# Optimization experiments

Hardware: AMD Instinct MI355X
Metric: run time of the kernel (lower is better)

The kernel has to match this reference:

```python
import jax, jax.numpy as jnp
import numpy as np

LEAK = 0.95
THRESHOLD = 1.0
CLAMP = 3.0
LN_EPS = 1e-5


def setup_inputs() -> dict:
    key = jax.random.key(0)
    k1, k2 = jax.random.split(key)
    B, S, V, D = 8, 2048, 57344, 1536
    token_ids = jax.random.randint(k1, (B, S), 0, V, dtype=jnp.int64)
    emb_table = jax.random.normal(k2, (V, D), dtype=jnp.float32) * 0.02
    gamma = jnp.ones((D,), dtype=jnp.float32)
    beta = jnp.zeros((D,), dtype=jnp.float32)
    return {"token_ids": token_ids, "emb_table": emb_table, "gamma": gamma, "beta": beta}


def _layernorm(x, gamma, beta):
    mu = jnp.mean(x, axis=-1, keepdims=True)
    var = jnp.mean(jnp.square(x - mu), axis=-1, keepdims=True)
    return (x - mu) * jax.lax.rsqrt(var + LN_EPS) * gamma + beta


def _lif_scan(x):
    # x: [B, S, D]; sequential LIF recurrence over time axis S
    B, S, D = x.shape
    v0 = jnp.zeros((B, D), dtype=x.dtype)

    def step(v, xt):
        v = v * LEAK + xt
        v = jnp.clip(v, -CLAMP, CLAMP)
        spike = (v >= THRESHOLD).astype(x.dtype)
        return v * (1.0 - spike), spike

    _, spikes = jax.lax.scan(step, v0, jnp.swapaxes(x, 0, 1))  # spikes: [S, B, D]
    return jnp.swapaxes(spikes, 0, 1)


def reference(token_ids, emb_table, gamma, beta):
    x = emb_table[token_ids]          # [B, S, D] embedding lookup
    x = _layernorm(x, gamma, beta)    # continuous residual stream
    spikes = _lif_scan(x)             # 0/1 spike tensor [B, S, D]
    return spikes, x
```

## Files before the change

kernel.cpp:

```cpp
#include <hip/hip_runtime.h>


constexpr int Bv = 8, Sv = 2048, Dv = 1536;
constexpr int Cn = 16;
constexpr int Ln = Sv / Cn;
constexpr int Wn = 64;
constexpr int BD = Bv * Dv;
constexpr int TNMAX = Ln + Wn;

constexpr size_t FLAG_OFF  = 0;
constexpr size_t STATS_OFF = 64;
constexpr size_t SPEC0_OFF = STATS_OFF + (size_t)2 * Bv * Sv * 8;
constexpr size_t SPEC1_OFF = SPEC0_OFF + (size_t)Cn * BD * 8;
constexpr size_t WS_NEED   = SPEC1_OFF + (size_t)Cn * BD * 8;

__device__ __forceinline__ double ln_x64(float e, double mu, double rs,
                                         double gd, double bd) {
#pragma clang fp contract(off)
    return (((double)e - mu) * rs) * gd + bd;
}
__device__ __forceinline__ double lif_step(double v, double x, bool& spike) {
#pragma clang fp contract(off)
    double vv = v * 0.95;
    vv = vv + x;
    vv = fmin(fmax(vv, -3.0), 3.0);
    spike = (vv >= 1.0);
    return spike ? 0.0 : vv;
}

extern "C" __global__ __launch_bounds__(256)
void detect_tok64(const int* __restrict__ tok, int* __restrict__ flag)
{
    __shared__ int any_nz;
    if (threadIdx.x == 0) any_nz = 0;
    __syncthreads();
    int nz = 0;
    for (int i = threadIdx.x; i < (Bv * Sv) / 2; i += 256) nz |= tok[2 * i + 1];
    if (nz) atomicOr(&any_nz, 1);
    __syncthreads();
    if (threadIdx.x == 0) flag[0] = (any_nz == 0) ? 1 : 0;
}

extern "C" __global__ __launch_bounds__(128)
void ln_stats_kernel(const int* __restrict__ tok,
                     const float* __restrict__ emb,
                     const float* __restrict__ gamma,
                     const float* __restrict__ beta,
                     float* __restrict__ x_out,
                     double* __restrict__ stats,
                     const int* __restrict__ tok64_flag)
{
#pragma clang fp contract(off)
    __shared__ double p1[2], p2[2];

    const int row = blockIdx.x;
    const int t   = threadIdx.x;
    const int lane = t & 63, wave = t >> 6;

    const int shift = tok64_flag[0];
    const long long tk = (long long)tok[(size_t)row << shift];
    const float* src = emb + tk * (long long)Dv;

    float4 xv[3];
#pragma unroll
    for (int k = 0; k < 3; ++k) xv[k] = reinterpret_cast<const float4*>(src)[t + 128 * k];

    double s = 0.0;
#pragma unroll
    for (int k = 0; k < 3; ++k) {
        s += (double)xv[k].x; s += (double)xv[k].y;
        s += (double)xv[k].z; s += (double)xv[k].w;
    }
#pragma unroll
    for (int off = 1; off < 64; off <<= 1) s += __shfl_xor(s, off);
    if (lane == 0) p1[wave] = s;
    __syncthreads();
    const double mu = (p1[0] + p1[1]) / 1536.0;

    double q = 0.0;
#pragma unroll
    for (int k = 0; k < 3; ++k) {
        double d0 = (double)xv[k].x - mu; q += d0 * d0;
        double d1 = (double)xv[k].y - mu; q += d1 * d1;
        double d2 = (double)xv[k].z - mu; q += d2 * d2;
        double d3 = (double)xv[k].w - mu; q += d3 * d3;
    }
#pragma unroll
    for (int off = 1; off < 64; off <<= 1) q += __shfl_xor(q, off);
    if (lane == 0) p2[wave] = q;
    __syncthreads();
    const double var  = (p2[0] + p2[1]) / 1536.0;
    const double rstd = 1.0 / sqrt(var + 1e-5);

    if (t == 0) { stats[2 * row] = mu; stats[2 * row + 1] = rstd; }

    float* dst = x_out + (long long)row * Dv;
#pragma unroll
    for (int k = 0; k < 3; ++k) {
        const int f4 = t + 128 * k;
        const float4 g4 = reinterpret_cast<const float4*>(gamma)[f4];
        const float4 b4 = reinterpret_cast<const float4*>(beta)[f4];
        float4 o;
        o.x = (float)((((double)xv[k].x - mu) * rstd) * (double)g4.x + (double)b4.x);
        o.y = (float)((((double)xv[k].y - mu) * rstd) * (double)g4.y + (double)b4.y);
        o.z = (float)((((double)xv[k].z - mu) * rstd) * (double)g4.z + (double)b4.z);
        o.w = (float)((((double)xv[k].w - mu) * rstd) * (double)g4.w + (double)b4.w);
        reinterpret_cast<float4*>(dst)[f4] = o;
    }
}

extern "C" __global__ __launch_bounds__(256)
void lif64_spec(const int* __restrict__ tok,
                const float* __restrict__ emb,
                const float* __restrict__ gamma,
                const float* __restrict__ beta,
                const double* __restrict__ stats,
                float* __restrict__ spk,
                double* __restrict__ spec_start,
                double* __restrict__ spec_end,
                const int* __restrict__ tok64_flag)
{
    constexpr int DBLK = Dv / 256;
    __shared__ int     tokl[TNMAX];
    __shared__ double2 statl[TNMAX];

    const int t    = threadIdx.x;
    const int bid  = blockIdx.x;
    const int dblk = bid % DBLK;
    const int c    = (bid / DBLK) % Cn;
    const int b    = bid / (DBLK * Cn);
    const int d    = dblk * 256 + t;

    const int s0 = c * Ln;
    const int sw = (c == 0) ? 0 : s0 - Wn;
    const int TN = s0 + Ln - sw;
    const int warm = s0 - sw;
    const int rowbase = b * Sv;

    if (t < TN) {
        const int row = rowbase + sw + t;
        const int shift = tok64_flag[0];
        tokl[t]  = tok[(size_t)row << shift];
        statl[t] = reinterpret_cast<const double2*>(stats)[row];
    }
    __syncthreads();

    const double gd = (double)gamma[d];
    const double bd = (double)beta[d];
    float* sp = spk + (size_t)b * Sv * Dv + d;

    constexpr int U = 16;
    float ecur[U], enxt[U];
#pragma unroll
    for (int k = 0; k < U; ++k)
        ecur[k] = emb[(long long)tokl[k] * Dv + d];

    double v = 0.0, vstart = 0.0;
    for (int i = 0; i < TN; i += U) {
        if (i + U < TN) {
#pragma unroll
            for (int k = 0; k < U; ++k)
                enxt[k] = emb[(long long)tokl[i + U + k] * Dv + d];
        }
#pragma unroll
        for (int k = 0; k < U; ++k) {
            const int idx = i + k;
            if (idx == warm) vstart = v;
            const double2 st = statl[idx];
            const double x = ln_x64(ecur[k], st.x, st.y, gd, bd);
            bool spike;
            const double vn = lif_step(v, x, spike);
            if (idx >= warm)
                __builtin_nontemporal_store(spike ? 1.0f : 0.0f,
                                            &sp[(size_t)(sw + idx) * Dv]);
            v = vn;
        }
#pragma unroll
        for (int k = 0; k < U; ++k) ecur[k] = enxt[k];
    }

    const size_t chain = (size_t)b * Dv + d;
    spec_start[(size_t)c * BD + chain] = vstart;
    spec_end[(size_t)c * BD + chain]   = v;
}

extern "C" __global__ __launch_bounds__(64)
void lif64_fixup(const int* __restrict__ tok,
                 const float* __restrict__ emb,
                 const float* __restrict__ gamma,
                 const float* __restrict__ beta,
                 const double* __restrict__ stats,
                 const double* __restrict__ spec_start,
                 const double* __restrict__ spec_end,
                 float* __restrict__ spk,
                 const int* __restrict__ tok64_flag)
{
    const int gid = blockIdx.x * 64 + threadIdx.x;
    const int b = gid / Dv;
    const int d = gid - b * Dv;
    const int shift = tok64_flag[0];
    const double gd = (double)gamma[d];
    const double bd = (double)beta[d];
    const int rowbase = b * Sv;
    float* sp = spk + (size_t)b * Sv * Dv + d;

    double v = 0.0;
    for (int c = 0; c < Cn; ++c) {
        const double vs = spec_start[(size_t)c * BD + gid];
        const double ve = spec_end[(size_t)c * BD + gid];
        if (v == vs) { v = ve; continue; }
        for (int s = c * Ln; s < c * Ln + Ln; ++s) {
            const int row = rowbase + s;
            const long long tk = (long long)tok[(size_t)row << shift];
            const float e = emb[tk * (long long)Dv + d];
            const double x = ln_x64(e, stats[2 * row], stats[2 * row + 1], gd, bd);
            bool spike;
            v = lif_step(v, x, spike);
            sp[(size_t)s * Dv] = spike ? 1.0f : 0.0f;
        }
    }
}

extern "C" __global__ __launch_bounds__(64)
void lif64_seq(const int* __restrict__ tok,
               const float* __restrict__ emb,
               const float* __restrict__ gamma,
               const float* __restrict__ beta,
               const double* __restrict__ stats,
               float* __restrict__ spk,
               const int* __restrict__ tok64_flag)
{
    const int gid = blockIdx.x * 64 + threadIdx.x;
    const int b = gid / Dv;
    const int d = gid - b * Dv;
    const int shift = tok64_flag[0];
    const int rowbase = b * Sv;
    const double gd = (double)gamma[d];
    const double bd = (double)beta[d];
    float* sp = spk + (size_t)b * Sv * Dv + d;

    constexpr int U = 8;
    float  ecur[U], enxt[U];
    double mcur[U], mnxt[U], rcur[U], rnxt[U];
#pragma unroll
    for (int k = 0; k < U; ++k) {
        const int row = rowbase + k;
        const long long tk = (long long)tok[(size_t)row << shift];
        ecur[k] = emb[tk * (long long)Dv + d];
        mcur[k] = stats[2 * row];
        rcur[k] = stats[2 * row + 1];
    }
    double v = 0.0;
    for (int s = 0; s < Sv; s += U) {
        if (s + U < Sv) {
#pragma unroll
            for (int k = 0; k < U; ++k) {
                const int row = rowbase + s + U + k;
                const long long tk = (long long)tok[(size_t)row << shift];
                enxt[k] = emb[tk * (long long)Dv + d];
                mnxt[k] = stats[2 * row];
                rnxt[k] = stats[2 * row + 1];
            }
        }
#pragma unroll
        for (int k = 0; k < U; ++k) {
            const double x = ln_x64(ecur[k], mcur[k], rcur[k], gd, bd);
            bool spike;
            v = lif_step(v, x, spike);
            __builtin_nontemporal_store(spike ? 1.0f : 0.0f, &sp[(size_t)(s + k) * Dv]);
        }
#pragma unroll
        for (int k = 0; k < U; ++k) { ecur[k] = enxt[k]; mcur[k] = mnxt[k]; rcur[k] = rnxt[k]; }
    }
}

extern "C" void kernel_launch(void* const* d_in, const int* in_sizes, int n_in,
                              void* d_out, int out_size, void* d_ws, size_t ws_size,
                              hipStream_t stream)
{
    const int*   tok   = (const int*)  d_in[0];
    const float* emb   = (const float*)d_in[1];
    const float* gamma = (const float*)d_in[2];
    const float* beta  = (const float*)d_in[3];

    float* out = (float*)d_out;
    float* spk = out;
    float* x   = out + (size_t)Bv * Sv * Dv;

    int*    flg   = (int*)((char*)d_ws + FLAG_OFF);
    double* stats = (double*)((char*)d_ws + STATS_OFF);

    detect_tok64<<<1, 256, 0, stream>>>(tok, flg);
    ln_stats_kernel<<<Bv * Sv, 128, 0, stream>>>(tok, emb, gamma, beta, x, stats, flg);

    if (ws_size >= WS_NEED) {
        double* spec0 = (double*)((char*)d_ws + SPEC0_OFF);
        double* spec1 = (double*)((char*)d_ws + SPEC1_OFF);
        lif64_spec<<<Bv * Cn * (Dv / 256), 256, 0, stream>>>(
            tok, emb, gamma, beta, stats, spk, spec0, spec1, flg);
        lif64_fixup<<<BD / 64, 64, 0, stream>>>(
            tok, emb, gamma, beta, stats, spec0, spec1, spk, flg);
    } else {
        lif64_seq<<<BD / 64, 64, 0, stream>>>(tok, emb, gamma, beta, stats, spk, flg);
    }
}
```

Baseline: 145.2 us.

## Double chunk count and software-prefetch gathers in the fixup pass

Raises the number of speculative time chunks from 16 to 32, which shortens each chunk's sequential scan and gives more parallel work. It also halves the register prefetch depth in the speculative kernel. The mismatch-repair kernel now prefetches 8 steps of embedding gathers and LN stats ahead, instead of loading them serially per step. More chunks mean a larger warm-up overhead relative to chunk length, more workspace for speculative states, and more chunk boundaries where speculation can miss.

```diff
diff --git a/kernel.cpp b/kernel.cpp
--- a/kernel.cpp
+++ b/kernel.cpp
@@ -2,7 +2,7 @@
 
 
 constexpr int Bv = 8, Sv = 2048, Dv = 1536;
-constexpr int Cn = 16;
+constexpr int Cn = 32;
 constexpr int Ln = Sv / Cn;
 constexpr int Wn = 64;
 constexpr int BD = Bv * Dv;
@@ -149,7 +149,7 @@
     const double bd = (double)beta[d];
     float* sp = spk + (size_t)b * Sv * Dv + d;
 
-    constexpr int U = 16;
+    constexpr int U = 8;
     float ecur[U], enxt[U];
 #pragma unroll
     for (int k = 0; k < U; ++k)
@@ -209,14 +209,40 @@
         const double vs = spec_start[(size_t)c * BD + gid];
         const double ve = spec_end[(size_t)c * BD + gid];
         if (v == vs) { v = ve; continue; }
-        for (int s = c * Ln; s < c * Ln + Ln; ++s) {
-            const int row = rowbase + s;
+        constexpr int U = 8;
+        const int s0 = c * Ln;
+        float  ecur[U], enxt[U];
+        double mcur[U], mnxt[U], rcur[U], rnxt[U];
+#pragma unroll
+        for (int k = 0; k < U; ++k) {
+            const int row = rowbase + s0 + k;
             const long long tk = (long long)tok[(size_t)row << shift];
-            const float e = emb[tk * (long long)Dv + d];
-            const double x = ln_x64(e, stats[2 * row], stats[2 * row + 1], gd, bd);
-            bool spike;
-            v = lif_step(v, x, spike);
-            sp[(size_t)s * Dv] = spike ? 1.0f : 0.0f;
+            ecur[k] = emb[tk * (long long)Dv + d];
+            mcur[k] = stats[2 * row];
+            rcur[k] = stats[2 * row + 1];
+        }
+        for (int i = 0; i < Ln; i += U) {
+            if (i + U < Ln) {
+#pragma unroll
+                for (int k = 0; k < U; ++k) {
+                    const int row = rowbase + s0 + i + U + k;
+                    const long long tk = (long long)tok[(size_t)row << shift];
+                    enxt[k] = emb[tk * (long long)Dv + d];
+                    mnxt[k] = stats[2 * row];
+                    rnxt[k] = stats[2 * row + 1];
+                }
+            }
+#pragma unroll
+            for (int k = 0; k < U; ++k) {
+                const double x = ln_x64(ecur[k], mcur[k], rcur[k], gd, bd);
+                bool spike;
+                v = lif_step(v, x, spike);
+                sp[(size_t)(s0 + i + k) * Dv] = spike ? 1.0f : 0.0f;
+            }
+#pragma unroll
+            for (int k = 0; k < U; ++k) {
+                ecur[k] = enxt[k]; mcur[k] = mnxt[k]; rcur[k] = rnxt[k];
+            }
         }
     }
 }
```

After: 118.9 us. 18.1% less time.
